# Kernel tuning notes

Measured on AMD Instinct MI355X. Metric: run time of the kernel, lower is better.

Reference implementation:

```python
import jax, jax.numpy as jnp
import numpy as np

D_MODEL, D_HIDDEN, N_EXPERTS = 1024, 4096, 8
CAP_FACTOR, LBL_COEF, ZLOSS_COEF = 1.25, 0.01, 0.0


def setup_inputs() -> dict:
    key = jax.random.key(0)
    ks = jax.random.split(key, 4)
    B, T = 4, 2048
    x = jax.random.normal(ks[0], (B, T, D_MODEL), dtype=jnp.float32)
    # router linear
    Wr = jax.random.normal(ks[1], (D_MODEL, N_EXPERTS), jnp.float32) / np.sqrt(D_MODEL).astype(np.float32)
    br = jnp.zeros((N_EXPERTS,), jnp.float32)
    # per-expert MLP: fc1 [D->H], gelu, fc2 [H->D]
    W1 = jax.random.normal(ks[2], (N_EXPERTS, D_MODEL, D_HIDDEN), jnp.float32) / np.sqrt(D_MODEL).astype(np.float32)
    b1 = jnp.zeros((N_EXPERTS, D_HIDDEN), jnp.float32)
    W2 = jax.random.normal(ks[3], (N_EXPERTS, D_HIDDEN, D_MODEL), jnp.float32) / np.sqrt(D_HIDDEN).astype(np.float32)
    b2 = jnp.zeros((N_EXPERTS, D_MODEL), jnp.float32)
    return {"x": x, "Wr": Wr, "br": br, "W1": W1, "b1": b1, "W2": W2, "b2": b2}


def reference(x, Wr, br, W1, b1, W2, b2):
    B, T, D = x.shape
    N = B * T
    E = Wr.shape[1]
    cap = int(CAP_FACTOR * (N / E) + 1)  # static Python int

    h = x.reshape(N, D)
    # --- Top1Router ---
    logits = h @ Wr + br                              # [N, E]
    probs = jax.nn.softmax(logits, axis=-1)
    top1 = jnp.argmax(probs, axis=-1)                 # [N]
    w = jnp.take_along_axis(probs, top1[:, None], axis=1)  # [N, 1]
    assign = jax.nn.one_hot(top1, E, dtype=jnp.float32)    # constant wrt grads
    importance = probs.mean(axis=0)
    load = jax.lax.stop_gradient(assign).mean(axis=0)
    lb_loss = E * jnp.sum(importance * load)
    z_loss = jnp.mean(jax.nn.logsumexp(logits, axis=-1) ** 2)

    # --- capacity-based dispatch (first `cap` tokens per expert, token order) ---
    pos = (jnp.cumsum(assign, axis=0) * assign).sum(axis=-1).astype(jnp.int32) - 1  # [N] slot within expert
    keep = pos < cap
    slot = jnp.where(keep, pos, cap)  # dropped tokens -> overflow slot `cap`
    xe = jnp.zeros((E, cap + 1, D), x.dtype).at[top1, slot].set(h)[:, :cap]  # [E, cap, D]

    # --- per-expert MLP as grouped GEMMs ---
    he = jax.nn.gelu(jnp.einsum('ecd,edh->ech', xe, W1) + b1[:, None, :])    # [E, cap, H]
    ye = jnp.einsum('ech,ehd->ecd', he, W2) + b2[:, None, :]                 # [E, cap, D]

    # --- combine (gather back, scale by router weight, zero dropped) ---
    out = ye[top1, jnp.minimum(pos, cap - 1)] * w   # [N, D]
    out = jnp.where(keep[:, None], out, jnp.zeros((), x.dtype))
    y = out.reshape(B, T, D)
    aux = LBL_COEF * lb_loss + ZLOSS_COEF * z_loss
    return (y, aux)
```

## Files before the change

kernel.cpp:

```cpp
#include <hip/hip_runtime.h>
#include <hip/hip_bf16.h>

#define N_TOK 8192
#define DM    1024
#define DH    4096
#define NE    8
#define CAP   1281
#define CAPR  1408
#define ISTR  1536

typedef unsigned short u16;
typedef __attribute__((ext_vector_type(8))) __bf16 bf16x8;
typedef __attribute__((ext_vector_type(8))) short short8;
typedef __attribute__((ext_vector_type(4))) short s16x4;
typedef __attribute__((ext_vector_type(4))) float f4;

__device__ __forceinline__ u16 f2bf(float f){
  union { float f; unsigned u; } v; v.f = f;
  unsigned r = v.u + 0x7fffu + ((v.u >> 16) & 1u);
  return (u16)(r >> 16);
}

__device__ __forceinline__ float gelu_fast(float v){
  float u = 0.7978845608028654f * (v + 0.044715f * v * v * v);
  return v * __builtin_amdgcn_rcpf(1.0f + __expf(-2.0f * u));
}

__device__ __forceinline__ void gl2lds16(const void* g, void* l){
  __builtin_amdgcn_global_load_lds((const __attribute__((address_space(1))) void*)g,
                                   (__attribute__((address_space(3))) void*)l, 16, 0, 0);
}

__device__ __forceinline__ void tcvt_tile(const float* __restrict__ ip, u16* __restrict__ op,
                                          int K, int Nn, int n0, int k0, int tt, float* tile){
  int kr = tt>>4, nc = (tt&15)*4;
  #pragma unroll
  for (int ii=0;ii<4;ii++){
    f4 v = *(const f4*)&ip[(size_t)(k0+kr+16*ii)*Nn + n0 + nc];
    float* row = &tile[(kr+16*ii)*65 + nc];
    row[0]=v[0]; row[1]=v[1]; row[2]=v[2]; row[3]=v[3];
  }
  __syncthreads();
  int nr = tt>>2, kc = (tt&3)*16;
  short8 o0, o1;
  #pragma unroll
  for (int c=0;c<8;c++){
    o0[c] = (short)f2bf(tile[(kc+c)*65 + nr]);
    o1[c] = (short)f2bf(tile[(kc+8+c)*65 + nr]);
  }
  *(short8*)&op[(size_t)(n0+nr)*K + k0 + kc] = o0;
  *(short8*)&op[(size_t)(n0+nr)*K + k0 + kc + 8] = o1;
}

__global__ __launch_bounds__(256) void rt_k(const float* __restrict__ x, const float* __restrict__ Wr,
    const float* __restrict__ br, u16* __restrict__ Xb, int* __restrict__ top1,
    float* __restrict__ wgt, float* __restrict__ pPart,
    const float* __restrict__ W1, u16* __restrict__ W1T){
  __shared__ float shbuf[64*65];
  int bid = blockIdx.x;
  if (bid >= 2048){
    int local = bid - 2048;
    int bx = local & 63, by = (local >> 6) & 15, bz = local >> 10;
    size_t mb = (size_t)bz * (size_t)DM * (size_t)DH;
    tcvt_tile(W1 + mb, W1T + mb, DM, DH, bx*64, by*64, threadIdx.x, shbuf);
    return;
  }
  float (*pSh)[8] = (float(*)[8])shbuf;
  int wid = threadIdx.x >> 6, lane = threadIdx.x & 63;
  int n = bid * 4 + wid;
  const float* xr = x + (size_t)n * DM;
  u16* xbr = Xb + (size_t)n * DM;
  float acc[8];
  #pragma unroll
  for (int e=0;e<8;e++) acc[e]=0.f;
  #pragma unroll
  for (int c=0;c<4;c++){
    int d0 = c*256 + lane*4;
    f4 xv = *(const f4*)(xr + d0);
    s16x4 xb;
    #pragma unroll
    for (int j=0;j<4;j++) xb[j] = (short)f2bf(xv[j]);
    *(s16x4*)(xbr + d0) = xb;
    #pragma unroll
    for (int j=0;j<4;j++){
      const float* wrow = Wr + (size_t)(d0+j)*NE;
      float xs = xv[j];
      #pragma unroll
      for (int e=0;e<8;e++) acc[e] = fmaf(xs, wrow[e], acc[e]);
    }
  }
  #pragma unroll
  for (int off=32; off>0; off>>=1){
    #pragma unroll
    for (int e=0;e<8;e++) acc[e] += __shfl_down(acc[e], off, 64);
  }
  if (lane==0){
    float lg[8]; float mx = -1e30f;
    #pragma unroll
    for (int e=0;e<8;e++){ lg[e] = acc[e] + br[e]; mx = fmaxf(mx, lg[e]); }
    float p[8], s=0.f;
    #pragma unroll
    for (int e=0;e<8;e++){ p[e] = expf(lg[e]-mx); s += p[e]; }
    int bt=0; float bv=lg[0];
    #pragma unroll
    for (int e=1;e<8;e++){ if (lg[e]>bv){ bv=lg[e]; bt=e; } }
    float inv = 1.f/s;
    top1[n] = bt; wgt[n] = p[bt]*inv;
    #pragma unroll
    for (int e=0;e<8;e++) pSh[wid][e] = p[e]*inv;
  }
  __syncthreads();
  if (threadIdx.x < 8){
    int e = threadIdx.x;
    pPart[bid*8 + e] = pSh[0][e]+pSh[1][e]+pSh[2][e]+pSh[3][e];
  }
}

__global__ __launch_bounds__(1024) void scan_k(const int* __restrict__ top1, int* __restrict__ idx,
    int* __restrict__ cnt, const float* __restrict__ pPart,
    float* __restrict__ y, float* __restrict__ auxOut){
  __shared__ int waveCnt[16][8];
  __shared__ int wavePre[16][8];
  __shared__ int chunkTot[8];
  __shared__ int base_s[8];
  __shared__ int dropLds[6912];
  __shared__ int nDropSh;
  __shared__ float impLds[8];
  int tid = threadIdx.x, wid = tid>>6, lane = tid&63;
  if (tid < 8){ base_s[tid] = 0; impLds[tid] = 0.f; }
  if (tid == 0) nDropSh = 0;
  __syncthreads();
  for (int c=0;c<8;c++){
    int t = c*1024 + tid;
    int e = top1[t];
    int myPre = 0;
    #pragma unroll
    for (int ex=0; ex<8; ex++){
      unsigned long long mk = __ballot(e == ex);
      if (lane == 0) waveCnt[wid][ex] = __popcll(mk);
      if (ex == e) myPre = __popcll(mk & ((1ull<<lane)-1ull));
    }
    __syncthreads();
    if (tid < 8){
      int run = 0;
      for (int wv=0; wv<16; wv++){ wavePre[wv][tid] = run; run += waveCnt[wv][tid]; }
      chunkTot[tid] = run;
    }
    __syncthreads();
    int pos = base_s[e] + wavePre[wid][e] + myPre;
    if (pos < CAP) idx[e*ISTR + pos] = t;
    else { int d = atomicAdd(&nDropSh, 1); dropLds[d] = t; }
    __syncthreads();
    if (tid < 8) base_s[tid] += chunkTot[tid];
    __syncthreads();
  }
  if (tid < 8) cnt[tid] = base_s[tid] < CAP ? base_s[tid] : CAP;
  {
    int e = tid & 7, bg = tid >> 3;
    float ps = 0.f;
    for (int b = bg; b < 2048; b += 128) ps += pPart[b*8 + e];
    atomicAdd(&impLds[e], ps);
  }
  __syncthreads();
  if (tid == 0){
    float s = 0.f;
    for (int e=0;e<8;e++) s += (impLds[e]*(1.f/N_TOK)) * ((float)base_s[e]*(1.f/N_TOK));
    *auxOut = 0.01f * 8.f * s;
  }
  int nd = nDropSh;
  for (int i=0; i<nd; i++){
    int t = dropLds[i];
    if (tid < 256){
      f4 z; z[0]=0.f; z[1]=0.f; z[2]=0.f; z[3]=0.f;
      *(f4*)&y[(size_t)t*DM + tid*4] = z;
    }
  }
}

#define LDA(buf, m, kk) (*(const bf16x8*)&lds[(buf)*16384 + (aBase ^ ((kk)*32)) + (m)*1024])
#define LDB(buf, n, kk) (*(const bf16x8*)&lds[32768 + (buf)*16384 + (bBase ^ ((kk)*32)) + (n)*1024])

#define SA_J(buf, j, kc) gl2lds16(aS[j] + (size_t)(kc)*64, &lds[(buf)*16384 + ((j)*512 + t)*8])
#define SB_ALLM(buf, kc) do{ \
  gl2lds16(bS[0] + (size_t)(kc)*64, &lds[32768 + (buf)*16384 + (0*512 + t)*8]); \
  gl2lds16(bS[1] + (size_t)(kc)*64, &lds[32768 + (buf)*16384 + (1*512 + t)*8]); \
  gl2lds16(bS[2] + (size_t)(kc)*64, &lds[32768 + (buf)*16384 + (2*512 + t)*8]); \
  gl2lds16(bS[3] + (size_t)(kc)*64, &lds[32768 + (buf)*16384 + (3*512 + t)*8]); }while(0)

#define SB0 __builtin_amdgcn_sched_barrier(0)
#define LGKM(n) do{ asm volatile("s_waitcnt lgkmcnt(" #n ")" ::: "memory"); SB0; }while(0)

#define READ_A(dst, mbase, buf) do{ \
  dst[0][0]=LDA(buf,(mbase),0);   dst[0][1]=LDA(buf,(mbase),1); \
  dst[1][0]=LDA(buf,(mbase)+1,0); dst[1][1]=LDA(buf,(mbase)+1,1); }while(0)

#define MFMA_PAIR(q, A_) \
  _Pragma("unroll") for (int j_=0;j_<2;j_++) \
    _Pragma("unroll") for (int n_=0;n_<4;n_++) \
      _Pragma("unroll") for (int kk_=0;kk_<2;kk_++) \
        acc[2*(q)+j_][n_] = __builtin_amdgcn_mfma_f32_16x16x32_bf16(A_[j_][kk_], Bf[n_][kk_], acc[2*(q)+j_][n_], 0,0,0);

#define KTILE(buf, ktv, NTv) do{ \
  int kc1 = (ktv)+1 < (NTv) ? (ktv)+1 : (NTv)-1; \
  int kc2 = (ktv)+2 < (NTv) ? (ktv)+2 : (NTv)-1; \
  asm volatile("s_waitcnt vmcnt(6)" ::: "memory"); \
  __builtin_amdgcn_s_barrier(); \
  SA_J((buf)^1, 1, kc1); SA_J((buf)^1, 3, kc1); \
  _Pragma("unroll") for (int n_=0;n_<4;n_++){ Bf[n_][0] = LDB(buf,n_,0); Bf[n_][1] = LDB(buf,n_,1); } \
  READ_A(aA, 0, buf); \
  SB0; \
  READ_A(aB, 2, buf); \
  LGKM(4); \
  __builtin_amdgcn_s_setprio(1); MFMA_PAIR(0, aA); __builtin_amdgcn_s_setprio(0); \
  __builtin_amdgcn_s_barrier(); \
  SB_ALLM(buf, kc2); \
  READ_A(aA, 4, buf); \
  LGKM(4); \
  __builtin_amdgcn_s_setprio(1); MFMA_PAIR(1, aB); __builtin_amdgcn_s_setprio(0); \
  __builtin_amdgcn_s_barrier(); \
  SA_J(buf, 0, kc2); SA_J(buf, 2, kc2); \
  READ_A(aB, 6, buf); \
  LGKM(4); \
  __builtin_amdgcn_s_setprio(1); MFMA_PAIR(2, aA); __builtin_amdgcn_s_setprio(0); \
  __builtin_amdgcn_s_barrier(); \
  LGKM(0); \
  __builtin_amdgcn_s_setprio(1); MFMA_PAIR(3, aB); __builtin_amdgcn_s_setprio(0); \
}while(0)

#define GEMM_PROLOGUE() do{ \
  SB_ALLM(0, 0); \
  SA_J(0,0,0); SA_J(0,2,0); \
  SA_J(0,1,0); SA_J(0,3,0); \
  SB_ALLM(1, 1); \
  SA_J(1,0,1); SA_J(1,2,1); }while(0)

__global__ __launch_bounds__(512, 2) void gemm1_k(
    const u16* __restrict__ Xb, const u16* __restrict__ W1T,
    const float* __restrict__ b1, const int* __restrict__ idx,
    const int* __restrict__ cnt, u16* __restrict__ He,
    const float* __restrict__ W2, u16* __restrict__ W2T)
{
  __shared__ __align__(16) u16 lds[65536];
  int bid = blockIdx.x;
  int t = threadIdx.x;
  if (bid >= 768){
    int half = t >> 8, tt = t & 255;
    int tau = (bid - 768)*2 + half;
    int bx = tau & 15, by = (tau >> 4) & 63, bz = tau >> 10;
    size_t mb = (size_t)bz * (size_t)DH * (size_t)DM;
    float* tile = ((float*)lds) + half*4160;
    tcvt_tile(W2 + mb, W2T + mb, DH, DM, bx*64, by*64, tt, tile);
    return;
  }
  int x = bid & 7, k = bid >> 3;
  int g = x*16 + k/6;
  int ntS = k - (k/6)*6;
  int e = g >> 4, mtH = g & 15;
  int cn = cnt[e];
  if (ntS*256 >= cn) return;
  int lane = t&63, wid = t>>6;
  int waveM = wid>>2, waveN = wid&3;
  int rA = lane&15, kb = lane>>4, s = rA&7;

  const u16* aS[4]; const u16* bS[4];
  #pragma unroll
  for (int j=0;j<4;j++){
    int pos = j*512 + t;
    int row = pos>>3, ch = pos&7;
    int gcb = ch ^ (row&7);
    aS[j] = W1T + ((size_t)e*DH + mtH*256 + row)*DM + gcb*8;
    int slotrow = ntS*256 + row;
    int token = (slotrow < cn) ? idx[e*ISTR + slotrow] : 0;
    bS[j] = Xb + (size_t)token*DM + gcb*8;
  }
  f4 acc[8][4];
  #pragma unroll
  for (int m=0;m<8;m++)
    #pragma unroll
    for (int n=0;n<4;n++)
      #pragma unroll
      for (int j=0;j<4;j++) acc[m][n][j]=0.f;

  int aBase = (waveM*128 + rA)*64 + (kb ^ s)*8;
  int bBase = (waveN*64  + rA)*64 + (kb ^ s)*8;
  bf16x8 Bf[4][2], aA[2][2], aB[2][2];

  GEMM_PROLOGUE();
  const int NT = DM/64;
  #pragma unroll 1
  for (int i=0;i<NT/2;i++){
    KTILE(0, 2*i,   NT);
    KTILE(1, 2*i+1, NT);
  }
  asm volatile("s_waitcnt vmcnt(0) lgkmcnt(0)" ::: "memory");

  int rG = lane>>4;
  #pragma unroll
  for (int m=0;m<8;m++){
    int h0 = mtH*256 + waveM*128 + m*16 + rG*4;
    f4 b4 = *(const f4*)&b1[e*DH + h0];
    #pragma unroll
    for (int n=0;n<4;n++){
      int slot = ntS*256 + waveN*64 + n*16 + rA;
      if (slot < cn){
        s16x4 v;
        #pragma unroll
        for (int j=0;j<4;j++) v[j] = (short)f2bf(gelu_fast(acc[m][n][j] + b4[j]));
        *(s16x4*)&He[((size_t)e*CAPR + slot)*DH + h0] = v;
      }
    }
  }
}

__global__ __launch_bounds__(512, 2) void gemm2_k(
    const u16* __restrict__ He, const u16* __restrict__ W2T,
    const float* __restrict__ b2, const int* __restrict__ idx,
    const int* __restrict__ cnt, const float* __restrict__ wgt,
    float* __restrict__ y)
{
  int bid = blockIdx.x;
  int x = bid & 7, k = bid >> 3;
  int g = x*4 + k/6;
  int mt = k - (k/6)*6;
  int e = g >> 2, nt = g & 3;
  int cn = cnt[e];
  if (mt*256 >= cn) return;
  __shared__ __align__(16) u16 lds[65536];
  int t = threadIdx.x, lane = t&63, wid = t>>6;
  int waveM = wid>>2, waveN = wid&3;
  int rA = lane&15, kb = lane>>4, s = rA&7;

  const u16* aS[4]; const u16* bS[4];
  #pragma unroll
  for (int j=0;j<4;j++){
    int pos = j*512 + t;
    int row = pos>>3, ch = pos&7;
    int gcb = ch ^ (row&7);
    int srow = mt*256 + row; if (srow >= cn) srow = cn-1;
    aS[j] = He  + ((size_t)e*CAPR + srow)*DH + gcb*8;
    bS[j] = W2T + ((size_t)e*DM + nt*256 + row)*DH + gcb*8;
  }
  f4 acc[8][4];
  #pragma unroll
  for (int m=0;m<8;m++)
    #pragma unroll
    for (int n=0;n<4;n++)
      #pragma unroll
      for (int j=0;j<4;j++) acc[m][n][j]=0.f;

  int aBase = (waveM*128 + rA)*64 + (kb ^ s)*8;
  int bBase = (waveN*64  + rA)*64 + (kb ^ s)*8;
  bf16x8 Bf[4][2], aA[2][2], aB[2][2];

  GEMM_PROLOGUE();
  const int NT = DH/64;
  #pragma unroll 1
  for (int i=0;i<NT/2;i++){
    KTILE(0, 2*i,   NT);
    KTILE(1, 2*i+1, NT);
  }
  asm volatile("s_waitcnt vmcnt(0) lgkmcnt(0)" ::: "memory");

  int rG = lane>>4;
  float bias_[4];
  #pragma unroll
  for (int n=0;n<4;n++) bias_[n] = b2[e*DM + nt*256 + waveN*64 + n*16 + rA];
  #pragma unroll
  for (int m=0;m<8;m++){
    int slot0 = mt*256 + waveM*128 + m*16 + rG*4;
    #pragma unroll
    for (int j=0;j<4;j++){
      int slot = slot0 + j;
      bool valid = slot < cn;
      int tk = valid ? idx[e*ISTR + slot] : 0;
      float wv = valid ? wgt[tk] : 0.f;
      float* yr = y + (size_t)tk*DM;
      #pragma unroll
      for (int n=0;n<4;n++){
        int col = nt*256 + waveN*64 + n*16 + rA;
        if (valid) yr[col] = (acc[m][n][j] + bias_[n]) * wv;
      }
    }
  }
}

extern "C" void kernel_launch(void* const* d_in, const int* in_sizes, int n_in,
                              void* d_out, int out_size, void* d_ws, size_t ws_size,
                              hipStream_t stream){
  const float* x  = (const float*)d_in[0];
  const float* Wr = (const float*)d_in[1];
  const float* br = (const float*)d_in[2];
  const float* W1 = (const float*)d_in[3];
  const float* b1 = (const float*)d_in[4];
  const float* W2 = (const float*)d_in[5];
  const float* b2 = (const float*)d_in[6];
  float* y = (float*)d_out;

  char* ws = (char*)d_ws;
  u16* Xb  = (u16*)(ws);
  u16* W1T = (u16*)(ws + 16777216ull);
  u16* W2T = (u16*)(ws + 16777216ull + 67108864ull);
  u16* He  = (u16*)(ws + 16777216ull + 2ull*67108864ull);
  char* tail = ws + 16777216ull + 2ull*67108864ull + (size_t)NE*CAPR*DH*2ull;
  int*   top1   = (int*)(tail);
  float* wgt    = (float*)(tail + 32768);
  int*   idx    = (int*)(tail + 65536);
  float* pPart  = (float*)(tail + 65536 + 49152);
  int*   cnt    = (int*)(tail + 65536 + 49152 + 65536);

  rt_k<<<2048 + 8192, 256, 0, stream>>>(x, Wr, br, Xb, top1, wgt, pPart, W1, W1T);
  scan_k<<<1, 1024, 0, stream>>>(top1, idx, cnt, pPart, y, y + (size_t)N_TOK*DM);
  gemm1_k<<<768 + 4096, 512, 0, stream>>>(Xb, W1T, b1, idx, cnt, He, W2, W2T);
  gemm2_k<<<192, 512, 0, stream>>>(He, W2T, b2, idx, cnt, wgt, y);

  (void)in_sizes; (void)n_in; (void)out_size; (void)ws_size;
}
```

Before: 329.8 us.

## Restructure GEMM main loop into eight-phase ping-pong schedule with half-tile prefetch

Replaces the four-phase K-tile macro with an eight-phase schedule covering two K tiles. Each phase loads its A fragments, issues half of one operand's global-to-LDS prefetch, then does a barrier and a full lgkmcnt wait before its MFMA block. The change spreads global loads more evenly across phases and simplifies the wait counts, and it applies to both expert GEMMs. In exchange it adds more barriers per tile and drops the partial lgkmcnt overlap between LDS reads and MFMAs, so some latency hiding may be lost.

```diff
diff --git a/kernel.cpp b/kernel.cpp
--- a/kernel.cpp
+++ b/kernel.cpp
@@ -177,62 +177,62 @@
   }
 }
 
+
 #define LDA(buf, m, kk) (*(const bf16x8*)&lds[(buf)*16384 + (aBase ^ ((kk)*32)) + (m)*1024])
 #define LDB(buf, n, kk) (*(const bf16x8*)&lds[32768 + (buf)*16384 + (bBase ^ ((kk)*32)) + (n)*1024])
 
-#define SA_J(buf, j, kc) gl2lds16(aS[j] + (size_t)(kc)*64, &lds[(buf)*16384 + ((j)*512 + t)*8])
-#define SB_ALLM(buf, kc) do{ \
-  gl2lds16(bS[0] + (size_t)(kc)*64, &lds[32768 + (buf)*16384 + (0*512 + t)*8]); \
-  gl2lds16(bS[1] + (size_t)(kc)*64, &lds[32768 + (buf)*16384 + (1*512 + t)*8]); \
-  gl2lds16(bS[2] + (size_t)(kc)*64, &lds[32768 + (buf)*16384 + (2*512 + t)*8]); \
-  gl2lds16(bS[3] + (size_t)(kc)*64, &lds[32768 + (buf)*16384 + (3*512 + t)*8]); }while(0)
+#define SA_H(buf, h, kc) do{ \
+  gl2lds16(aS[2*(h)]   + (size_t)(kc)*64, &lds[(buf)*16384 + ((2*(h))*512   + t)*8]); \
+  gl2lds16(aS[2*(h)+1] + (size_t)(kc)*64, &lds[(buf)*16384 + ((2*(h)+1)*512 + t)*8]); }while(0)
+#define SB_H(buf, h, kc) do{ \
+  gl2lds16(bS[2*(h)]   + (size_t)(kc)*64, &lds[32768 + (buf)*16384 + ((2*(h))*512   + t)*8]); \
+  gl2lds16(bS[2*(h)+1] + (size_t)(kc)*64, &lds[32768 + (buf)*16384 + ((2*(h)+1)*512 + t)*8]); }while(0)
 
 #define SB0 __builtin_amdgcn_sched_barrier(0)
-#define LGKM(n) do{ asm volatile("s_waitcnt lgkmcnt(" #n ")" ::: "memory"); SB0; }while(0)
-
-#define READ_A(dst, mbase, buf) do{ \
-  dst[0][0]=LDA(buf,(mbase),0);   dst[0][1]=LDA(buf,(mbase),1); \
-  dst[1][0]=LDA(buf,(mbase)+1,0); dst[1][1]=LDA(buf,(mbase)+1,1); }while(0)
-
-#define MFMA_PAIR(q, A_) \
+#define VMC(n) asm volatile("s_waitcnt vmcnt(" #n ")" ::: "memory")
+
+#define PHASE8(buf, q, STAGE, DOVM) do{ \
+  bf16x8 a_[2][2]; \
+  if ((q)==0){ \
+    _Pragma("unroll") for (int n_=0;n_<4;n_++){ Bf[n_][0]=LDB(buf,n_,0); Bf[n_][1]=LDB(buf,n_,1); } \
+  } \
+  a_[0][0]=LDA(buf,2*(q),0);   a_[0][1]=LDA(buf,2*(q),1); \
+  a_[1][0]=LDA(buf,2*(q)+1,0); a_[1][1]=LDA(buf,2*(q)+1,1); \
+  STAGE; \
+  SB0; \
+  __builtin_amdgcn_s_barrier(); \
+  asm volatile("s_waitcnt lgkmcnt(0)" ::: "memory"); \
+  SB0; \
+  __builtin_amdgcn_s_setprio(1); \
   _Pragma("unroll") for (int j_=0;j_<2;j_++) \
     _Pragma("unroll") for (int n_=0;n_<4;n_++) \
       _Pragma("unroll") for (int kk_=0;kk_<2;kk_++) \
-        acc[2*(q)+j_][n_] = __builtin_amdgcn_mfma_f32_16x16x32_bf16(A_[j_][kk_], Bf[n_][kk_], acc[2*(q)+j_][n_], 0,0,0);
-
-#define KTILE(buf, ktv, NTv) do{ \
-  int kc1 = (ktv)+1 < (NTv) ? (ktv)+1 : (NTv)-1; \
-  int kc2 = (ktv)+2 < (NTv) ? (ktv)+2 : (NTv)-1; \
-  asm volatile("s_waitcnt vmcnt(6)" ::: "memory"); \
+        acc[2*(q)+j_][n_] = __builtin_amdgcn_mfma_f32_16x16x32_bf16(a_[j_][kk_], Bf[n_][kk_], acc[2*(q)+j_][n_], 0,0,0); \
+  __builtin_amdgcn_s_setprio(0); \
+  DOVM; \
   __builtin_amdgcn_s_barrier(); \
-  SA_J((buf)^1, 1, kc1); SA_J((buf)^1, 3, kc1); \
-  _Pragma("unroll") for (int n_=0;n_<4;n_++){ Bf[n_][0] = LDB(buf,n_,0); Bf[n_][1] = LDB(buf,n_,1); } \
-  READ_A(aA, 0, buf); \
-  SB0; \
-  READ_A(aB, 2, buf); \
-  LGKM(4); \
-  __builtin_amdgcn_s_setprio(1); MFMA_PAIR(0, aA); __builtin_amdgcn_s_setprio(0); \
-  __builtin_amdgcn_s_barrier(); \
-  SB_ALLM(buf, kc2); \
-  READ_A(aA, 4, buf); \
-  LGKM(4); \
-  __builtin_amdgcn_s_setprio(1); MFMA_PAIR(1, aB); __builtin_amdgcn_s_setprio(0); \
-  __builtin_amdgcn_s_barrier(); \
-  SA_J(buf, 0, kc2); SA_J(buf, 2, kc2); \
-  READ_A(aB, 6, buf); \
-  LGKM(4); \
-  __builtin_amdgcn_s_setprio(1); MFMA_PAIR(2, aA); __builtin_amdgcn_s_setprio(0); \
-  __builtin_amdgcn_s_barrier(); \
-  LGKM(0); \
-  __builtin_amdgcn_s_setprio(1); MFMA_PAIR(3, aB); __builtin_amdgcn_s_setprio(0); \
 }while(0)
 
-#define GEMM_PROLOGUE() do{ \
-  SB_ALLM(0, 0); \
-  SA_J(0,0,0); SA_J(0,2,0); \
-  SA_J(0,1,0); SA_J(0,3,0); \
-  SB_ALLM(1, 1); \
-  SA_J(1,0,1); SA_J(1,2,1); }while(0)
+#define KTILE2(ii, NTv) do{ \
+  int kt1 = 2*(ii)+1 < (NTv) ? 2*(ii)+1 : (NTv)-1; \
+  int kt2 = 2*(ii)+2 < (NTv) ? 2*(ii)+2 : (NTv)-1; \
+  int kt3 = 2*(ii)+3 < (NTv) ? 2*(ii)+3 : (NTv)-1; \
+  PHASE8(0,0, SA_H(1,0,kt1), (void)0); \
+  PHASE8(0,1, SA_H(1,1,kt1), (void)0); \
+  PHASE8(0,2, SB_H(0,0,kt2), (void)0); \
+  PHASE8(0,3, SB_H(0,1,kt2), VMC(4)); \
+  PHASE8(1,0, SA_H(0,0,kt2), (void)0); \
+  PHASE8(1,1, SA_H(0,1,kt2), (void)0); \
+  PHASE8(1,2, SB_H(1,0,kt3), (void)0); \
+  PHASE8(1,3, SB_H(1,1,kt3), VMC(4)); \
+}while(0)
+
+#define GEMM_PROLOGUE8() do{ \
+  SB_H(0,0,0); SB_H(0,1,0); \
+  SA_H(0,0,0); SA_H(0,1,0); \
+  SB_H(1,0,1); SB_H(1,1,1); \
+  VMC(4); \
+  __builtin_amdgcn_s_barrier(); }while(0)
 
 __global__ __launch_bounds__(512, 2) void gemm1_k(
     const u16* __restrict__ Xb, const u16* __restrict__ W1T,
@@ -283,14 +283,13 @@
 
   int aBase = (waveM*128 + rA)*64 + (kb ^ s)*8;
   int bBase = (waveN*64  + rA)*64 + (kb ^ s)*8;
-  bf16x8 Bf[4][2], aA[2][2], aB[2][2];
-
-  GEMM_PROLOGUE();
+  bf16x8 Bf[4][2];
+
+  GEMM_PROLOGUE8();
   const int NT = DM/64;
   #pragma unroll 1
   for (int i=0;i<NT/2;i++){
-    KTILE(0, 2*i,   NT);
-    KTILE(1, 2*i+1, NT);
+    KTILE2(i, NT);
   }
   asm volatile("s_waitcnt vmcnt(0) lgkmcnt(0)" ::: "memory");
 
@@ -350,14 +349,13 @@
 
   int aBase = (waveM*128 + rA)*64 + (kb ^ s)*8;
   int bBase = (waveN*64  + rA)*64 + (kb ^ s)*8;
-  bf16x8 Bf[4][2], aA[2][2], aB[2][2];
-
-  GEMM_PROLOGUE();
+  bf16x8 Bf[4][2];
+
+  GEMM_PROLOGUE8();
   const int NT = DH/64;
   #pragma unroll 1
   for (int i=0;i<NT/2;i++){
-    KTILE(0, 2*i,   NT);
-    KTILE(1, 2*i+1, NT);
+    KTILE2(i, NT);
   }
   asm volatile("s_waitcnt vmcnt(0) lgkmcnt(0)" ::: "memory");
 
```

After: 335.1 us. No clear change (+1.6%).
